# Kernel tuning notes

Hardware: AMD Instinct MI355X
Metric: run time of the kernel (lower is better)

## Reference

```python
import jax, jax.numpy as jnp
import numpy as np
import math

D_MODEL = 1024
N_HEADS = 16
D_FF = 4096
D_K = D_MODEL // N_HEADS
B, S = 2, 2048
EPS = 1e-5


def _linear_params(key, fan_in, fan_out):
    kw, kb = jax.random.split(key)
    bound = 1.0 / math.sqrt(fan_in)
    W = jax.random.uniform(kw, (fan_out, fan_in), jnp.float32, -bound, bound)
    b = jax.random.uniform(kb, (fan_out,), jnp.float32, -bound, bound)
    return W, b


def setup_inputs() -> dict:
    key = jax.random.key(0)
    ks = jax.random.split(key, 8)
    x = jax.random.normal(ks[0], (B, S, D_MODEL), jnp.float32)
    # causal mask, broadcast over batch and heads; 0 -> masked
    mask = jnp.tril(jnp.ones((S, S), jnp.int32))[None, None, :, :]
    wq, bq = _linear_params(ks[1], D_MODEL, D_MODEL)
    wk, bk = _linear_params(ks[2], D_MODEL, D_MODEL)
    wv, bv = _linear_params(ks[3], D_MODEL, D_MODEL)
    wo, bo = _linear_params(ks[4], D_MODEL, D_MODEL)
    w1, b1 = _linear_params(ks[5], D_MODEL, D_FF)
    w2, b2 = _linear_params(ks[6], D_FF, D_MODEL)
    g1 = jnp.ones((D_MODEL,), jnp.float32)
    be1 = jnp.zeros((D_MODEL,), jnp.float32)
    g2 = jnp.ones((D_MODEL,), jnp.float32)
    be2 = jnp.zeros((D_MODEL,), jnp.float32)
    return dict(x=x, mask=mask, wq=wq, bq=bq, wk=wk, bk=bk, wv=wv, bv=bv,
                wo=wo, bo=bo, w1=w1, b1=b1, w2=w2, b2=b2,
                g1=g1, be1=be1, g2=g2, be2=be2)


def _layernorm(x, g, b):
    mu = jnp.mean(x, axis=-1, keepdims=True)
    var = jnp.mean(jnp.square(x - mu), axis=-1, keepdims=True)
    return (x - mu) * jax.lax.rsqrt(var + EPS) * g + b


def reference(x, mask, wq, bq, wk, bk, wv, bv, wo, bo, w1, b1, w2, b2, g1, be1, g2, be2):
    Bsz, Sl, _ = x.shape
    def heads(t):  # [B,S,D] -> [B,H,S,d_k]
        return t.reshape(Bsz, Sl, N_HEADS, D_K).transpose(0, 2, 1, 3)
    Q = heads(x @ wq.T + bq)
    K = heads(x @ wk.T + bk)
    V = heads(x @ wv.T + bv)
    scores = jnp.einsum('bhqd,bhkd->bhqk', Q, K) / math.sqrt(D_K)
    scores = jnp.where(mask == 0, jnp.float32(-1e9), scores)
    attn = jax.nn.softmax(scores, axis=-1)
    out = jnp.einsum('bhqk,bhkd->bhqd', attn, V)
    out = out.transpose(0, 2, 1, 3).reshape(Bsz, Sl, D_MODEL)
    attn_out = out @ wo.T + bo
    h = _layernorm(x + attn_out, g1, be1)  # dropout is identity in eval
    ff = jax.nn.relu(h @ w1.T + b1) @ w2.T + b2
    return _layernorm(h + ff, g2, be2)
```

## Files before the change

### kernel.cpp

```cpp
#include <hip/hip_runtime.h>
#include <hip/hip_bf16.h>


using f32x4 = __attribute__((ext_vector_type(4))) float;
using s16x8 = __attribute__((ext_vector_type(8))) short;

constexpr int D_MODEL = 1024;
constexpr int D_FF    = 4096;
constexpr int DK      = 64;
constexpr int BB      = 2;
constexpr int SS      = 2048;
constexpr int NTOK    = BB * SS;

#define QSCALE 0.18033688011112042f

__device__ __forceinline__ ushort f2bf(float f) {
    unsigned u = __float_as_uint(f);
    u += 0x7fffu + ((u >> 16) & 1u);
    return (ushort)(u >> 16);
}

__device__ __forceinline__ float bflo(uint v) { return __uint_as_float(v << 16); }
__device__ __forceinline__ float bfhi(uint v) { return __uint_as_float(v & 0xffff0000u); }

__device__ __forceinline__ float ex2(float x) {
    float r;
    asm("v_exp_f32 %0, %1" : "=v"(r) : "v"(x));
    return r;
}

__device__ __forceinline__ void gload_lds16(const void* g, void* l) {
    __builtin_amdgcn_global_load_lds(
        (const __attribute__((address_space(1))) void*)g,
        (__attribute__((address_space(3))) void*)l, 16, 0, 0);
}

__device__ __forceinline__ void wait_vm4() {
    asm volatile("s_waitcnt vmcnt(4)" ::: "memory");
    __builtin_amdgcn_sched_barrier(0);
}
__device__ __forceinline__ void wait_vm0() {
    asm volatile("s_waitcnt vmcnt(0)" ::: "memory");
    __builtin_amdgcn_sched_barrier(0);
}
__device__ __forceinline__ void wait_lgkm0() {
    asm volatile("s_waitcnt lgkmcnt(0)" ::: "memory");
    __builtin_amdgcn_sched_barrier(0);
}

struct CvtArgs { const float* src[7]; ushort* dst[7]; };

__global__ __launch_bounds__(256) void cvt_all(CvtArgs a) {
    constexpr long S[8] = {0L<<20, 1L<<20, 2L<<20, 3L<<20,
                           4L<<20, 8L<<20, 12L<<20, 16L<<20};
    long i = ((long)blockIdx.x * 256 + threadIdx.x) * 4;
    int s = 0;
#pragma unroll
    for (int j = 1; j < 7; ++j) if (i >= S[j]) s = j;
    long off = i - S[s];
    float4 v = *(const float4*)(a.src[s] + off);
    ushort4 o;
    o.x = f2bf(v.x); o.y = f2bf(v.y); o.z = f2bf(v.z); o.w = f2bf(v.w);
    *(ushort4*)(a.dst[s] + off) = o;
}

__global__ __launch_bounds__(512, 2) void gemm256_relu(
        const ushort* __restrict__ A, const ushort* __restrict__ Wt,
        const float* __restrict__ bias, ushort* __restrict__ C,
        int M, int N, int K) {
    __shared__ __align__(16) char Als[2][2][128 * 128];
    __shared__ __align__(16) char Bls[2][2][128 * 128];

    const int nwg = (int)gridDim.x;
    const int id  = (int)blockIdx.x;
    const int sw  = (id & 7) * (nwg >> 3) + (id >> 3);
    const int gx  = N >> 8;
    const int bx  = sw % gx, by = sw / gx;
    const int bm0 = by << 8, bn0 = bx << 8;

    const int t  = threadIdx.x;
    const int l  = t & 63;
    const int w  = t >> 6;
    const int li = l & 15, g = l >> 4;
    const int wm = w >> 2, wn = w & 3;

    const int srow  = w * 8 + (l >> 3);
    const int scolb = (l & 7) * 16;
    const int svz   = (scolb ^ ((srow & 7) << 4)) >> 1;
    const int nk    = K >> 6;

    auto stA = [&](int buf, int half, int kt) {
        if (kt >= nk) return;
        const ushort* src = A + (size_t)(bm0 + half * 128 + srow) * K + kt * 64 + svz;
        char* dst = Als[buf][half] + w * 1024;
        gload_lds16(src, dst);
        gload_lds16(src + (size_t)64 * K, dst + 8192);
    };
    auto stB = [&](int buf, int half, int kt) {
        if (kt >= nk) return;
        const ushort* src = Wt + (size_t)(bn0 + half * 128 + srow) * K + kt * 64 + svz;
        char* dst = Bls[buf][half] + w * 1024;
        gload_lds16(src, dst);
        gload_lds16(src + (size_t)64 * K, dst + 8192);
    };

    const int rdsw = (li & 7) << 4;

    f32x4 acc[8][4];
#pragma unroll
    for (int m = 0; m < 8; ++m)
#pragma unroll
        for (int n = 0; n < 4; ++n)
            acc[m][n] = (f32x4){0.f, 0.f, 0.f, 0.f};

    auto ldA2 = [&](int buf, int q, s16x8 af[2][2]) {
#pragma unroll
        for (int m2 = 0; m2 < 2; ++m2)
#pragma unroll
            for (int kk = 0; kk < 2; ++kk)
                af[m2][kk] = *(const s16x8*)(Als[buf][wm] +
                    ((q * 2 + m2) * 16 + li) * 128 + ((kk * 64 + g * 16) ^ rdsw));
    };
    auto ldB8 = [&](int buf, s16x8 bfr[4][2]) {
#pragma unroll
        for (int nf = 0; nf < 4; ++nf)
#pragma unroll
            for (int kk = 0; kk < 2; ++kk)
                bfr[nf][kk] = *(const s16x8*)(Bls[buf][wn >> 1] +
                    ((wn & 1) * 64 + nf * 16 + li) * 128 + ((kk * 64 + g * 16) ^ rdsw));
    };
    auto mfmaq = [&](int q, s16x8 af[2][2], s16x8 bfr[4][2], int wm_mode) {
        __builtin_amdgcn_s_barrier();
        wait_lgkm0();
        __builtin_amdgcn_s_setprio(1);
#pragma unroll
        for (int m2 = 0; m2 < 2; ++m2)
#pragma unroll
            for (int nf = 0; nf < 4; ++nf)
#pragma unroll
            for (int kk = 0; kk < 2; ++kk)
                acc[q * 2 + m2][nf] = __builtin_amdgcn_mfma_f32_16x16x32_bf16(
                    af[m2][kk], bfr[nf][kk], acc[q * 2 + m2][nf], 0, 0, 0);
        __builtin_amdgcn_s_setprio(0);
        if (wm_mode == 4) wait_vm4();
        else if (wm_mode == 0) wait_vm0();
        __builtin_amdgcn_s_barrier();
    };

    stB(0, 0, 0); stB(0, 1, 0);
    stA(0, 0, 0); stA(0, 1, 0);
    stB(1, 0, 1); stB(1, 1, 1);
    wait_vm4();
    __builtin_amdgcn_s_barrier();

    const int ni = nk >> 1;
    for (int i = 0; i < ni; ++i) {
        const int t0 = 2 * i;
        const bool last = (i == ni - 1);
        {
            s16x8 bfr[4][2];
            { ldB8(0, bfr); s16x8 af[2][2]; ldA2(0, 0, af);
              stA(1, 0, t0 + 1);                      mfmaq(0, af, bfr, -1); }
            { s16x8 af[2][2]; ldA2(0, 1, af);
              stA(1, 1, t0 + 1); stB(0, 0, t0 + 2);   mfmaq(1, af, bfr, -1); }
            { s16x8 af[2][2]; ldA2(0, 2, af);
              stB(0, 1, t0 + 2);                      mfmaq(2, af, bfr, -1); }
            { s16x8 af[2][2]; ldA2(0, 3, af);
                                                      mfmaq(3, af, bfr, last ? 0 : 4); }
        }
        {
            s16x8 bfr[4][2];
            { ldB8(1, bfr); s16x8 af[2][2]; ldA2(1, 0, af);
              stA(0, 0, t0 + 2);                      mfmaq(0, af, bfr, -1); }
            { s16x8 af[2][2]; ldA2(1, 1, af);
              stA(0, 1, t0 + 2);                      mfmaq(1, af, bfr, -1); }
            { s16x8 af[2][2]; ldA2(1, 2, af);
              stB(1, 0, t0 + 3);                      mfmaq(2, af, bfr, -1); }
            { s16x8 af[2][2]; ldA2(1, 3, af);
              stB(1, 1, t0 + 3);
                                                      mfmaq(3, af, bfr, last ? -1 : 4); }
        }
    }

#pragma unroll
    for (int mf = 0; mf < 8; ++mf) {
        int row0 = bm0 + wm * 128 + mf * 16 + g * 4;
#pragma unroll
        for (int nf = 0; nf < 4; ++nf) {
            int col = bn0 + wn * 64 + nf * 16 + li;
            float bsv = bias[col];
#pragma unroll
            for (int r = 0; r < 4; ++r) {
                float v = fmaxf(acc[mf][nf][r] + bsv, 0.f);
                C[(size_t)(row0 + r) * N + col] = f2bf(v);
            }
        }
    }
}

__global__ __launch_bounds__(512, 2) void gemm256_psum(
        const ushort* __restrict__ A, const ushort* __restrict__ Wt,
        const float* __restrict__ bias, ushort* __restrict__ Cout,
        int M, int N, int Klen, int ldk, int splitk) {
    __shared__ __align__(16) char Als[2][2][128 * 128];
    __shared__ __align__(16) char Bls[2][2][128 * 128];

    const int nwg = (int)gridDim.x;
    const int id  = (int)blockIdx.x;
    const int sw  = (id & 7) * (nwg >> 3) + (id >> 3);
    const int gx  = N >> 8;
    const int tps = nwg / splitk;
    const int s   = sw / tps;
    const int rem = sw - s * tps;
    const int bx  = rem % gx, by = rem / gx;
    const int bm0 = by << 8, bn0 = bx << 8;
    const int kbase = s * Klen;

    const int t  = threadIdx.x;
    const int l  = t & 63;
    const int w  = t >> 6;
    const int li = l & 15, g = l >> 4;
    const int wm = w >> 2, wn = w & 3;

    const int srow  = w * 8 + (l >> 3);
    const int scolb = (l & 7) * 16;
    const int svz   = (scolb ^ ((srow & 7) << 4)) >> 1;
    const int nk    = Klen >> 6;

    auto stA = [&](int buf, int half, int kt) {
        if (kt >= nk) return;
        const ushort* src = A + (size_t)(bm0 + half * 128 + srow) * ldk + kbase + kt * 64 + svz;
        char* dst = Als[buf][half] + w * 1024;
        gload_lds16(src, dst);
        gload_lds16(src + (size_t)64 * ldk, dst + 8192);
    };
    auto stB = [&](int buf, int half, int kt) {
        if (kt >= nk) return;
        const ushort* src = Wt + (size_t)(bn0 + half * 128 + srow) * ldk + kbase + kt * 64 + svz;
        char* dst = Bls[buf][half] + w * 1024;
        gload_lds16(src, dst);
        gload_lds16(src + (size_t)64 * ldk, dst + 8192);
    };

    const int rdsw = (li & 7) << 4;

    f32x4 acc[8][4];
#pragma unroll
    for (int m = 0; m < 8; ++m)
#pragma unroll
        for (int n = 0; n < 4; ++n)
            acc[m][n] = (f32x4){0.f, 0.f, 0.f, 0.f};

    auto ldA2 = [&](int buf, int q, s16x8 af[2][2]) {
#pragma unroll
        for (int m2 = 0; m2 < 2; ++m2)
#pragma unroll
            for (int kk = 0; kk < 2; ++kk)
                af[m2][kk] = *(const s16x8*)(Als[buf][wm] +
                    ((q * 2 + m2) * 16 + li) * 128 + ((kk * 64 + g * 16) ^ rdsw));
    };
    auto ldB8 = [&](int buf, s16x8 bfr[4][2]) {
#pragma unroll
        for (int nf = 0; nf < 4; ++nf)
#pragma unroll
            for (int kk = 0; kk < 2; ++kk)
                bfr[nf][kk] = *(const s16x8*)(Bls[buf][wn >> 1] +
                    ((wn & 1) * 64 + nf * 16 + li) * 128 + ((kk * 64 + g * 16) ^ rdsw));
    };
    auto mfmaq = [&](int q, s16x8 af[2][2], s16x8 bfr[4][2], int wm_mode) {
        __builtin_amdgcn_s_barrier();
        wait_lgkm0();
        __builtin_amdgcn_s_setprio(1);
#pragma unroll
        for (int m2 = 0; m2 < 2; ++m2)
#pragma unroll
            for (int nf = 0; nf < 4; ++nf)
#pragma unroll
            for (int kk = 0; kk < 2; ++kk)
                acc[q * 2 + m2][nf] = __builtin_amdgcn_mfma_f32_16x16x32_bf16(
                    af[m2][kk], bfr[nf][kk], acc[q * 2 + m2][nf], 0, 0, 0);
        __builtin_amdgcn_s_setprio(0);
        if (wm_mode == 4) wait_vm4();
        else if (wm_mode == 0) wait_vm0();
        __builtin_amdgcn_s_barrier();
    };

    stB(0, 0, 0); stB(0, 1, 0);
    stA(0, 0, 0); stA(0, 1, 0);
    stB(1, 0, 1); stB(1, 1, 1);
    wait_vm4();
    __builtin_amdgcn_s_barrier();

    const int ni = nk >> 1;
    for (int i = 0; i < ni; ++i) {
        const int t0 = 2 * i;
        const bool last = (i == ni - 1);
        {
            s16x8 bfr[4][2];
            { ldB8(0, bfr); s16x8 af[2][2]; ldA2(0, 0, af);
              stA(1, 0, t0 + 1);                      mfmaq(0, af, bfr, -1); }
            { s16x8 af[2][2]; ldA2(0, 1, af);
              stA(1, 1, t0 + 1); stB(0, 0, t0 + 2);   mfmaq(1, af, bfr, -1); }
            { s16x8 af[2][2]; ldA2(0, 2, af);
              stB(0, 1, t0 + 2);                      mfmaq(2, af, bfr, -1); }
            { s16x8 af[2][2]; ldA2(0, 3, af);
                                                      mfmaq(3, af, bfr, last ? 0 : 4); }
        }
        {
            s16x8 bfr[4][2];
            { ldB8(1, bfr); s16x8 af[2][2]; ldA2(1, 0, af);
              stA(0, 0, t0 + 2);                      mfmaq(0, af, bfr, -1); }
            { s16x8 af[2][2]; ldA2(1, 1, af);
              stA(0, 1, t0 + 2);                      mfmaq(1, af, bfr, -1); }
            { s16x8 af[2][2]; ldA2(1, 2, af);
              stB(1, 0, t0 + 3);                      mfmaq(2, af, bfr, -1); }
            { s16x8 af[2][2]; ldA2(1, 3, af);
              stB(1, 1, t0 + 3);
                                                      mfmaq(3, af, bfr, last ? -1 : 4); }
        }
    }

    const bool dobias = (s == 0);
    ushort* Cb = Cout + (size_t)s * M * N;
#pragma unroll
    for (int mf = 0; mf < 8; ++mf) {
        int row0 = bm0 + wm * 128 + mf * 16 + g * 4;
#pragma unroll
        for (int nf = 0; nf < 4; ++nf) {
            int col = bn0 + wn * 64 + nf * 16 + li;
            float bsv = dobias ? bias[col] : 0.f;
#pragma unroll
            for (int r = 0; r < 4; ++r) {
                float v = acc[mf][nf][r] + bsv;
                Cb[(size_t)(row0 + r) * N + col] = f2bf(v);
            }
        }
    }
}

__global__ __launch_bounds__(512, 2) void gemm256_qkvt(
        const ushort* __restrict__ xb, const ushort* __restrict__ wqkb,
        const ushort* __restrict__ wvb,
        const float* __restrict__ bq, const float* __restrict__ bk,
        const float* __restrict__ bv,
        ushort* __restrict__ QKb, ushort* __restrict__ VtG) {
    __shared__ __align__(16) char Als[2][2][128 * 128];
    __shared__ __align__(16) char Bls[2][2][128 * 128];

    const int id = (int)blockIdx.x;
    const int sw = (id & 7) * 24 + (id >> 3);
    const bool vt = (sw >= 128);
    const ushort *Aop, *Wop;
    int bm0, bn0;
    if (!vt) { bm0 = (sw >> 3) << 8;  bn0 = (sw & 7) << 8;          Aop = xb;  Wop = wqkb; }
    else     { int s2 = sw - 128; bm0 = (s2 >> 4) << 8; bn0 = (s2 & 15) << 8; Aop = wvb; Wop = xb; }

    const int t  = threadIdx.x;
    const int l  = t & 63;
    const int w  = t >> 6;
    const int li = l & 15, g = l >> 4;
    const int wm = w >> 2, wn = w & 3;

    const int srow  = w * 8 + (l >> 3);
    const int scolb = (l & 7) * 16;
    const int svz   = (scolb ^ ((srow & 7) << 4)) >> 1;
    constexpr int K = 1024, nk = 16;

    auto stA = [&](int buf, int half, int kt) {
        if (kt >= nk) return;
        const ushort* src = Aop + (size_t)(bm0 + half * 128 + srow) * K + kt * 64 + svz;
        char* dst = Als[buf][half] + w * 1024;
        gload_lds16(src, dst);
        gload_lds16(src + (size_t)64 * K, dst + 8192);
    };
    auto stB = [&](int buf, int half, int kt) {
        if (kt >= nk) return;
        const ushort* src = Wop + (size_t)(bn0 + half * 128 + srow) * K + kt * 64 + svz;
        char* dst = Bls[buf][half] + w * 1024;
        gload_lds16(src, dst);
        gload_lds16(src + (size_t)64 * K, dst + 8192);
    };

    const int rdsw = (li & 7) << 4;

    f32x4 acc[8][4];
#pragma unroll
    for (int m = 0; m < 8; ++m)
#pragma unroll
        for (int n = 0; n < 4; ++n)
            acc[m][n] = (f32x4){0.f, 0.f, 0.f, 0.f};

    auto ldA2 = [&](int buf, int q, s16x8 af[2][2]) {
#pragma unroll
        for (int m2 = 0; m2 < 2; ++m2)
#pragma unroll
            for (int kk = 0; kk < 2; ++kk)
                af[m2][kk] = *(const s16x8*)(Als[buf][wm] +
                    ((q * 2 + m2) * 16 + li) * 128 + ((kk * 64 + g * 16) ^ rdsw));
    };
    auto ldB8 = [&](int buf, s16x8 bfr[4][2]) {
#pragma unroll
        for (int nf = 0; nf < 4; ++nf)
#pragma unroll
            for (int kk = 0; kk < 2; ++kk)
                bfr[nf][kk] = *(const s16x8*)(Bls[buf][wn >> 1] +
                    ((wn & 1) * 64 + nf * 16 + li) * 128 + ((kk * 64 + g * 16) ^ rdsw));
    };
    auto mfmaq = [&](int q, s16x8 af[2][2], s16x8 bfr[4][2], int wm_mode) {
        __builtin_amdgcn_s_barrier();
        wait_lgkm0();
        __builtin_amdgcn_s_setprio(1);
#pragma unroll
        for (int m2 = 0; m2 < 2; ++m2)
#pragma unroll
            for (int nf = 0; nf < 4; ++nf)
#pragma unroll
            for (int kk = 0; kk < 2; ++kk)
                acc[q * 2 + m2][nf] = __builtin_amdgcn_mfma_f32_16x16x32_bf16(
                    af[m2][kk], bfr[nf][kk], acc[q * 2 + m2][nf], 0, 0, 0);
        __builtin_amdgcn_s_setprio(0);
        if (wm_mode == 4) wait_vm4();
        else if (wm_mode == 0) wait_vm0();
        __builtin_amdgcn_s_barrier();
    };

    stB(0, 0, 0); stB(0, 1, 0);
    stA(0, 0, 0); stA(0, 1, 0);
    stB(1, 0, 1); stB(1, 1, 1);
    wait_vm4();
    __builtin_amdgcn_s_barrier();

    const int ni = nk >> 1;
    for (int i = 0; i < ni; ++i) {
        const int t0 = 2 * i;
        const bool last = (i == ni - 1);
        {
            s16x8 bfr[4][2];
            { ldB8(0, bfr); s16x8 af[2][2]; ldA2(0, 0, af);
              stA(1, 0, t0 + 1);                      mfmaq(0, af, bfr, -1); }
            { s16x8 af[2][2]; ldA2(0, 1, af);
              stA(1, 1, t0 + 1); stB(0, 0, t0 + 2);   mfmaq(1, af, bfr, -1); }
            { s16x8 af[2][2]; ldA2(0, 2, af);
              stB(0, 1, t0 + 2);                      mfmaq(2, af, bfr, -1); }
            { s16x8 af[2][2]; ldA2(0, 3, af);
                                                      mfmaq(3, af, bfr, last ? 0 : 4); }
        }
        {
            s16x8 bfr[4][2];
            { ldB8(1, bfr); s16x8 af[2][2]; ldA2(1, 0, af);
              stA(0, 0, t0 + 2);                      mfmaq(0, af, bfr, -1); }
            { s16x8 af[2][2]; ldA2(1, 1, af);
              stA(0, 1, t0 + 2);                      mfmaq(1, af, bfr, -1); }
            { s16x8 af[2][2]; ldA2(1, 2, af);
              stB(1, 0, t0 + 3);                      mfmaq(2, af, bfr, -1); }
            { s16x8 af[2][2]; ldA2(1, 3, af);
              stB(1, 1, t0 + 3);
                                                      mfmaq(3, af, bfr, last ? -1 : 4); }
        }
    }

#pragma unroll
    for (int mf = 0; mf < 8; ++mf) {
        int row0 = bm0 + wm * 128 + mf * 16 + g * 4;
#pragma unroll
        for (int nf = 0; nf < 4; ++nf) {
            int col = bn0 + wn * 64 + nf * 16 + li;
            if (!vt) {
                float bsv = (col < 1024) ? bq[col] : bk[col - 1024];
                float sc  = (col < 1024) ? QSCALE : 1.f;
#pragma unroll
                for (int r = 0; r < 4; ++r) {
                    float v = (acc[mf][nf][r] + bsv) * sc;
                    QKb[(size_t)(row0 + r) * 2048 + col] = f2bf(v);
                }
            } else {
#pragma unroll
                for (int r = 0; r < 4; ++r) {
                    float v = acc[mf][nf][r] + bv[row0 + r];
                    VtG[(size_t)(row0 + r) * 4096 + col] = f2bf(v);
                }
            }
        }
    }
}

__global__ __launch_bounds__(256, 4) void attn_kernel(
        const ushort* __restrict__ QKb, const ushort* __restrict__ VtG,
        ushort* __restrict__ po, float* __restrict__ ml) {
    __shared__ __align__(16) char Ks[2][64 * 128];
    __shared__ __align__(16) char Vs[2][64 * 128];
    __shared__ __align__(16) char Ps[4][16 * 128];

    const int t  = threadIdx.x;
    const int l  = t & 63;
    const int w  = t >> 6;
    const int li = l & 15, g = l >> 4;

    const int id   = (int)blockIdx.x;
    const int xcd  = id & 7;
    const int rest = id >> 3;
    const int grp  = xcd + 8 * (rest >> 5);
    const int k32  = rest & 31;
    const int h    = grp >> 1;
    const int b    = grp & 1;
    const int bx   = k32 & 15;
    const int half = k32 >> 4;

    const ushort* Kp = QKb + (size_t)(b * SS) * 2048 + 1024 + h * DK;
    const ushort* Vp = VtG + (size_t)(h * DK) * NTOK + b * SS;

    const int rsub = l >> 3, slot = l & 7;
    const int swzsrc = (slot * 16) ^ (rsub << 4);

    auto stage = [&](int buf, int kt) {
#pragma unroll
        for (int c = 0; c < 2; ++c) {
            int row0 = (w + c * 4) * 8;
            gload_lds16((const char*)(Kp + (size_t)(kt + row0 + rsub) * 2048) + swzsrc,
                        Ks[buf] + row0 * 128);
            gload_lds16((const char*)(Vp + (size_t)(row0 + rsub) * NTOK + kt) + swzsrc,
                        Vs[buf] + row0 * 128);
        }
    };

    char* Pw = Ps[w];
    const int rswz = (li & 7) << 4;

    s16x8 vones;
#pragma unroll
    for (int j = 0; j < 8; ++j) vones[j] = (short)0x3F80;

    const int hi  = SS / 64 - 1 - bx;
    const int lo  = bx;
    const int qwH = hi * 64 + w * 16;
    const int qwL = lo * 64 + w * 16;

    s16x8 qfH[2], qfL[2];
    {
        const ushort* QpH = QKb + (size_t)(b * SS + qwH) * 2048 + h * DK;
        const ushort* QpL = QKb + (size_t)(b * SS + qwL) * 2048 + h * DK;
#pragma unroll
        for (int ds = 0; ds < 2; ++ds) {
            qfH[ds] = *(const s16x8*)(QpH + li * 2048 + ds * 32 + g * 8);
            qfL[ds] = *(const s16x8*)(QpL + li * 2048 + ds * 32 + g * 8);
        }
    }

    f32x4 oH[4], oL[4], osH, osL;
#pragma unroll
    for (int d = 0; d < 4; ++d) {
        oH[d] = (f32x4){0.f, 0.f, 0.f, 0.f};
        oL[d] = (f32x4){0.f, 0.f, 0.f, 0.f};
    }
    osH = (f32x4){0.f, 0.f, 0.f, 0.f};
    osL = (f32x4){0.f, 0.f, 0.f, 0.f};

    auto process = [&](const s16x8 (&qf)[2], f32x4 (&o)[4], f32x4& osum,
                       int j, int stripe, int qw, int cur) {
        const int kt = j * 64;
        f32x4 sa[4];
#pragma unroll
        for (int ks = 0; ks < 4; ++ks) sa[ks] = (f32x4){0.f, 0.f, 0.f, 0.f};
#pragma unroll
        for (int ks = 0; ks < 4; ++ks) {
            int row = ks * 16 + li;
#pragma unroll
            for (int ds = 0; ds < 2; ++ds) {
                s16x8 kf = *(const s16x8*)(Ks[cur] + row * 128 + ((ds * 64 + g * 16) ^ rswz));
                __builtin_amdgcn_s_setprio(1);
                sa[ks] = __builtin_amdgcn_mfma_f32_16x16x32_bf16(kf, qf[ds], sa[ks], 0, 0, 0);
                __builtin_amdgcn_s_setprio(0);
            }
        }

        const bool maskt = (j == stripe);
        float p[4][4];
#pragma unroll
        for (int ks = 0; ks < 4; ++ks)
#pragma unroll
            for (int r = 0; r < 4; ++r) {
                float sv = sa[ks][r];
                if (maskt && (kt + ks * 16 + g * 4 + r > qw + li)) sv = -1e30f;
                p[ks][r] = ex2(sv);
            }

#pragma unroll
        for (int ks = 0; ks < 4; ++ks) {
            uint u0, u1;
            asm("v_cvt_pk_bf16_f32 %0, %1, %2" : "=v"(u0) : "v"(p[ks][0]), "v"(p[ks][1]));
            asm("v_cvt_pk_bf16_f32 %0, %1, %2" : "=v"(u1) : "v"(p[ks][2]), "v"(p[ks][3]));
            uint2 uv; uv.x = u0; uv.y = u1;
            *(uint2*)(Pw + li * 128 + ((ks * 32 + g * 8) ^ rswz)) = uv;
        }

        s16x8 pf[2];
#pragma unroll
        for (int ks2 = 0; ks2 < 2; ++ks2)
            pf[ks2] = *(const s16x8*)(Pw + li * 128 + ((ks2 * 64 + g * 16) ^ rswz));
#pragma unroll
        for (int dblk = 0; dblk < 4; ++dblk) {
            int vrow = dblk * 16 + li;
#pragma unroll
            for (int ks2 = 0; ks2 < 2; ++ks2) {
                s16x8 vf = *(const s16x8*)(Vs[cur] + vrow * 128 + ((ks2 * 64 + g * 16) ^ rswz));
                __builtin_amdgcn_s_setprio(1);
                o[dblk] = __builtin_amdgcn_mfma_f32_16x16x32_bf16(pf[ks2], vf, o[dblk], 0, 0, 0);
                __builtin_amdgcn_s_setprio(0);
            }
        }
#pragma unroll
        for (int ks2 = 0; ks2 < 2; ++ks2)
            osum = __builtin_amdgcn_mfma_f32_16x16x32_bf16(pf[ks2], vones, osum, 0, 0, 0);
    };

    const int nt = ((hi - half) >> 1) + 1;
    stage(0, half * 64);
    __syncthreads();

    for (int it = 0; it < nt; ++it) {
        const int j   = half + 2 * it;
        const int cur = it & 1;
        if (it + 1 < nt) stage(cur ^ 1, j * 64 + 128);

        process(qfH, oH, osH, j, hi, qwH, cur);
        if (j <= lo)
            process(qfL, oL, osL, j, lo, qwL, cur);

        __syncthreads();
    }

#pragma unroll
    for (int r = 0; r < 4; ++r) {
        ushort* ppH = po + ((((size_t)(half * 2 + b)) * SS + qwH + g * 4 + r) * 16 + h) * 64;
        ushort* ppL = po + ((((size_t)(half * 2 + b)) * SS + qwL + g * 4 + r) * 16 + h) * 64;
#pragma unroll
        for (int dblk = 0; dblk < 4; ++dblk) {
            ppH[dblk * 16 + li] = f2bf(oH[dblk][r]);
            ppL[dblk * 16 + li] = f2bf(oL[dblk][r]);
        }
    }
    {
        const int qrow = l & 15;
        const int src  = (qrow >> 2) << 4;
        float tH0 = __shfl(osH[0], src), tH1 = __shfl(osH[1], src);
        float tH2 = __shfl(osH[2], src), tH3 = __shfl(osH[3], src);
        float tL0 = __shfl(osL[0], src), tL1 = __shfl(osL[1], src);
        float tL2 = __shfl(osL[2], src), tL3 = __shfl(osL[3], src);
        const int rr = qrow & 3;
        float lsH = rr == 0 ? tH0 : rr == 1 ? tH1 : rr == 2 ? tH2 : tH3;
        float lsL = rr == 0 ? tL0 : rr == 1 ? tL1 : rr == 2 ? tL2 : tL3;
        if (l < 16) {
            size_t mrowH = (((size_t)(half * 2 + b)) * SS + qwH + l) * 16 + h;
            ml[mrowH * 2]     = 0.f;
            ml[mrowH * 2 + 1] = lsH;
            size_t mrowL = (((size_t)(half * 2 + b)) * SS + qwL + l) * 16 + h;
            ml[mrowL * 2]     = 0.f;
            ml[mrowL * 2 + 1] = lsL;
        }
    }
}

__global__ __launch_bounds__(256) void attn_combine(
        const ushort* __restrict__ po, const float* __restrict__ ml,
        ushort* __restrict__ ctx) {
    const int idx = blockIdx.x * 256 + threadIdx.x;
    const int row = idx >> 4;
    const int d4  = (idx & 15) * 4;
    const int HR  = 2 * SS * 16;

    float m0 = ml[(size_t)row * 2],        l0 = ml[(size_t)row * 2 + 1];
    float m1 = ml[(size_t)(HR + row) * 2], l1 = ml[(size_t)(HR + row) * 2 + 1];
    float mx = fmaxf(m0, m1);
    float w0 = ex2(m0 - mx), w1 = ex2(m1 - mx);
    float inv = 1.0f / (l0 * w0 + l1 * w1);

    uint2 a = *(const uint2*)(po + (size_t)row * 64 + d4);
    uint2 c = *(const uint2*)(po + (size_t)(HR + row) * 64 + d4);
    float v0 = (bflo(a.x) * w0 + bflo(c.x) * w1) * inv;
    float v1 = (bfhi(a.x) * w0 + bfhi(c.x) * w1) * inv;
    float v2 = (bflo(a.y) * w0 + bflo(c.y) * w1) * inv;
    float v3 = (bfhi(a.y) * w0 + bfhi(c.y) * w1) * inv;
    ushort4 o;
    o.x = f2bf(v0); o.y = f2bf(v1); o.z = f2bf(v2); o.w = f2bf(v3);
    *(ushort4*)(ctx + (size_t)(row >> 4) * 1024 + (row & 15) * 64 + d4) = o;
}

template <bool WBF>
__global__ __launch_bounds__(256) void ln_fused(
        const float* __restrict__ xa, const ushort* __restrict__ pb,
        const float* __restrict__ gamma, const float* __restrict__ beta,
        float* __restrict__ outf, ushort* __restrict__ outb) {
    const int row = blockIdx.x;
    const int t   = threadIdx.x;
    const size_t off = (size_t)row * D_MODEL + t * 4;
    float4 a = *(const float4*)(xa + off);
    float z0 = a.x, z1 = a.y, z2 = a.z, z3 = a.w;
#pragma unroll
    for (int s = 0; s < 4; ++s) {
        uint2 c = *(const uint2*)(pb + (size_t)s * NTOK * D_MODEL + off);
        z0 += bflo(c.x); z1 += bfhi(c.x); z2 += bflo(c.y); z3 += bfhi(c.y);
    }
    float sum = z0 + z1 + z2 + z3;
    float sq  = z0 * z0 + z1 * z1 + z2 * z2 + z3 * z3;
#pragma unroll
    for (int o = 1; o < 64; o <<= 1) {
        sum += __shfl_xor(sum, o);
        sq  += __shfl_xor(sq, o);
    }
    __shared__ float s1[4], s2[4];
    if ((t & 63) == 0) { s1[t >> 6] = sum; s2[t >> 6] = sq; }
    __syncthreads();
    float tot = s1[0] + s1[1] + s1[2] + s1[3];
    float tsq = s2[0] + s2[1] + s2[2] + s2[3];
    const float invn = 1.0f / (float)D_MODEL;
    float mu  = tot * invn;
    float var = tsq * invn - mu * mu;
    float rstd = rsqrtf(var + 1e-5f);
    float4 gv = *(const float4*)(gamma + t * 4);
    float4 bv = *(const float4*)(beta + t * 4);
    float y0 = (z0 - mu) * rstd * gv.x + bv.x;
    float y1 = (z1 - mu) * rstd * gv.y + bv.y;
    float y2 = (z2 - mu) * rstd * gv.z + bv.z;
    float y3 = (z3 - mu) * rstd * gv.w + bv.w;
    float4 y = {y0, y1, y2, y3};
    *(float4*)(outf + off) = y;
    if constexpr (WBF) {
        ushort4 u;
        u.x = f2bf(y0); u.y = f2bf(y1); u.z = f2bf(y2); u.w = f2bf(y3);
        *(ushort4*)(outb + off) = u;
    }
}

extern "C" void kernel_launch(void* const* d_in, const int* in_sizes, int n_in,
                              void* d_out, int out_size, void* d_ws, size_t ws_size,
                              hipStream_t stream) {
    const float* x   = (const float*)d_in[0];
    const float* wq  = (const float*)d_in[2];  const float* bq  = (const float*)d_in[3];
    const float* wk  = (const float*)d_in[4];  const float* bk  = (const float*)d_in[5];
    const float* wv  = (const float*)d_in[6];  const float* bv  = (const float*)d_in[7];
    const float* wo  = (const float*)d_in[8];  const float* bo  = (const float*)d_in[9];
    const float* w1  = (const float*)d_in[10]; const float* b1  = (const float*)d_in[11];
    const float* w2  = (const float*)d_in[12]; const float* b2  = (const float*)d_in[13];
    const float* g1  = (const float*)d_in[14]; const float* be1 = (const float*)d_in[15];
    const float* g2  = (const float*)d_in[16]; const float* be2 = (const float*)d_in[17];
    float* out = (float*)d_out;

    char* ws = (char*)d_ws;
    const size_t MB = 1u << 20;
    ushort* wqkb = (ushort*)(ws + 0 * MB);
    ushort* wvb  = (ushort*)(ws + 4 * MB);
    ushort* wob  = (ushort*)(ws + 6 * MB);
    ushort* w1b  = (ushort*)(ws + 8 * MB);
    ushort* w2b  = (ushort*)(ws + 16 * MB);
    ushort* xb   = (ushort*)(ws + 24 * MB);
    ushort* QKb  = (ushort*)(ws + 32 * MB);
    ushort* VtG  = (ushort*)(ws + 48 * MB);
    ushort* ctx  = (ushort*)(ws + 56 * MB);
    ushort* po   = (ushort*)(ws + 64 * MB);
    float*  ml   = (float*)(ws + 81 * MB);
    ushort* p01  = (ushort*)(ws + 64 * MB);
    float*  h    = (float*)(ws + 96 * MB);
    ushort* hb   = (ushort*)(ws + 112 * MB);
    ushort* ffib = (ushort*)(ws + 24 * MB);

    CvtArgs ca;
    ca.src[0] = wq; ca.dst[0] = wqkb;
    ca.src[1] = wk; ca.dst[1] = wqkb + D_MODEL * D_MODEL;
    ca.src[2] = wv; ca.dst[2] = wvb;
    ca.src[3] = wo; ca.dst[3] = wob;
    ca.src[4] = w1; ca.dst[4] = w1b;
    ca.src[5] = w2; ca.dst[5] = w2b;
    ca.src[6] = x;  ca.dst[6] = xb;
    cvt_all<<<dim3(16384), dim3(256), 0, stream>>>(ca);

    gemm256_qkvt<<<dim3(192), dim3(512), 0, stream>>>(
        xb, wqkb, wvb, bq, bk, bv, QKb, VtG);

    attn_kernel<<<dim3(1024), dim3(256), 0, stream>>>(QKb, VtG, po, ml);
    attn_combine<<<dim3(4096), dim3(256), 0, stream>>>(po, ml, ctx);

    gemm256_psum<<<dim3(256), dim3(512), 0, stream>>>(
        ctx, wob, bo, p01, NTOK, D_MODEL, 256, D_MODEL, 4);
    ln_fused<true><<<dim3(NTOK), dim3(256), 0, stream>>>(x, p01, g1, be1, h, hb);

    gemm256_relu<<<dim3(256), dim3(512), 0, stream>>>(hb, w1b, b1, ffib, NTOK, D_FF, D_MODEL);

    gemm256_psum<<<dim3(256), dim3(512), 0, stream>>>(
        ffib, w2b, b2, p01, NTOK, D_MODEL, 1024, D_FF, 4);
    ln_fused<false><<<dim3(NTOK), dim3(256), 0, stream>>>(h, p01, g2, be2, out, nullptr);
}
```

Baseline: 216.1 us.

## Split V-transpose GEMM over K into two partial tiles and combine

The V^T tiles of the fused QKV GEMM are split along K into two halves, giving 256 blocks instead of 192 so the grid fills all CUs more evenly. Each half writes bf16 partials to a scratch buffer, and a new vt_combine kernel sums them into VtG. This adds a kernel launch and extra memory traffic (about 16MB read, 8MB written). It also rounds each partial to bf16 before the sum, which loses some precision.

```diff
diff --git a/kernel.cpp b/kernel.cpp
--- a/kernel.cpp
+++ b/kernel.cpp
@@ -343,17 +343,25 @@
         const ushort* __restrict__ wvb,
         const float* __restrict__ bq, const float* __restrict__ bk,
         const float* __restrict__ bv,
-        ushort* __restrict__ QKb, ushort* __restrict__ VtG) {
+        ushort* __restrict__ QKb, ushort* __restrict__ VtP) {
     __shared__ __align__(16) char Als[2][2][128 * 128];
     __shared__ __align__(16) char Bls[2][2][128 * 128];
 
     const int id = (int)blockIdx.x;
-    const int sw = (id & 7) * 24 + (id >> 3);
+    const int sw = (id & 7) * 32 + (id >> 3);
     const bool vt = (sw >= 128);
     const ushort *Aop, *Wop;
-    int bm0, bn0;
-    if (!vt) { bm0 = (sw >> 3) << 8;  bn0 = (sw & 7) << 8;          Aop = xb;  Wop = wqkb; }
-    else     { int s2 = sw - 128; bm0 = (s2 >> 4) << 8; bn0 = (s2 & 15) << 8; Aop = wvb; Wop = xb; }
+    int bm0, bn0, kbase, nk, vs = 0;
+    if (!vt) {
+        bm0 = (sw >> 3) << 8; bn0 = (sw & 7) << 8;
+        Aop = xb; Wop = wqkb; kbase = 0; nk = 16;
+    } else {
+        int s2 = sw - 128;
+        vs  = s2 >> 6;
+        int rem = s2 & 63;
+        bm0 = (rem >> 4) << 8; bn0 = (rem & 15) << 8;
+        Aop = wvb; Wop = xb; kbase = vs * 512; nk = 8;
+    }
 
     const int t  = threadIdx.x;
     const int l  = t & 63;
@@ -364,18 +372,18 @@
     const int srow  = w * 8 + (l >> 3);
     const int scolb = (l & 7) * 16;
     const int svz   = (scolb ^ ((srow & 7) << 4)) >> 1;
-    constexpr int K = 1024, nk = 16;
+    constexpr int K = 1024;
 
     auto stA = [&](int buf, int half, int kt) {
         if (kt >= nk) return;
-        const ushort* src = Aop + (size_t)(bm0 + half * 128 + srow) * K + kt * 64 + svz;
+        const ushort* src = Aop + (size_t)(bm0 + half * 128 + srow) * K + kbase + kt * 64 + svz;
         char* dst = Als[buf][half] + w * 1024;
         gload_lds16(src, dst);
         gload_lds16(src + (size_t)64 * K, dst + 8192);
     };
     auto stB = [&](int buf, int half, int kt) {
         if (kt >= nk) return;
-        const ushort* src = Wop + (size_t)(bn0 + half * 128 + srow) * K + kt * 64 + svz;
+        const ushort* src = Wop + (size_t)(bn0 + half * 128 + srow) * K + kbase + kt * 64 + svz;
         char* dst = Bls[buf][half] + w * 1024;
         gload_lds16(src, dst);
         gload_lds16(src + (size_t)64 * K, dst + 8192);
@@ -474,14 +482,30 @@
                     QKb[(size_t)(row0 + r) * 2048 + col] = f2bf(v);
                 }
             } else {
+                ushort* Vp = VtP + (size_t)vs * 1024 * 4096;
+                float bsv = (vs == 0) ? 0.f : 0.f;
 #pragma unroll
                 for (int r = 0; r < 4; ++r) {
-                    float v = acc[mf][nf][r] + bv[row0 + r];
-                    VtG[(size_t)(row0 + r) * 4096 + col] = f2bf(v);
+                    float v = acc[mf][nf][r] + (vs == 0 ? bv[row0 + r] : 0.f);
+                    Vp[(size_t)(row0 + r) * 4096 + col] = f2bf(v);
                 }
+                (void)bsv;
             }
         }
     }
+}
+
+__global__ __launch_bounds__(256) void vt_combine(
+        const ushort* __restrict__ VtP, ushort* __restrict__ VtG) {
+    const size_t i = ((size_t)blockIdx.x * 256 + threadIdx.x) * 4;
+    uint2 a = *(const uint2*)(VtP + i);
+    uint2 c = *(const uint2*)(VtP + (size_t)1024 * 4096 + i);
+    ushort4 o;
+    o.x = f2bf(bflo(a.x) + bflo(c.x));
+    o.y = f2bf(bfhi(a.x) + bfhi(c.x));
+    o.z = f2bf(bflo(a.y) + bflo(c.y));
+    o.w = f2bf(bfhi(a.y) + bfhi(c.y));
+    *(ushort4*)(VtG + i) = o;
 }
 
 __global__ __launch_bounds__(256, 4) void attn_kernel(
@@ -758,6 +782,7 @@
     ushort* ctx  = (ushort*)(ws + 56 * MB);
     ushort* po   = (ushort*)(ws + 64 * MB);
     float*  ml   = (float*)(ws + 81 * MB);
+    ushort* vtp  = (ushort*)(ws + 64 * MB);
     ushort* p01  = (ushort*)(ws + 64 * MB);
     float*  h    = (float*)(ws + 96 * MB);
     ushort* hb   = (ushort*)(ws + 112 * MB);
@@ -773,8 +798,9 @@
     ca.src[6] = x;  ca.dst[6] = xb;
     cvt_all<<<dim3(16384), dim3(256), 0, stream>>>(ca);
 
-    gemm256_qkvt<<<dim3(192), dim3(512), 0, stream>>>(
-        xb, wqkb, wvb, bq, bk, bv, QKb, VtG);
+    gemm256_qkvt<<<dim3(256), dim3(512), 0, stream>>>(
+        xb, wqkb, wvb, bq, bk, bv, QKb, vtp);
+    vt_combine<<<dim3(4096), dim3(256), 0, stream>>>(vtp, VtG);
 
     attn_kernel<<<dim3(1024), dim3(256), 0, stream>>>(QKb, VtG, po, ml);
     attn_combine<<<dim3(4096), dim3(256), 0, stream>>>(po, ml, ctx);
```

Result: slower. 223.2 us (+3.3%).
